# Performance work log

Measured on AMD Instinct MI355X. Metric: run time of the kernel, lower is better.

## Reference

```python
import jax, jax.numpy as jnp
import numpy as np

N, E = 100000, 1600000
IN_D, BOND_D, HID, OUT_D = 64, 16, 128, 64
COMB = 2 * IN_D + BOND_D + 1  # 145


def _mlp(h, W1, b1, W2, b2):
    # Linear -> SiLU -> Linear
    h = h @ W1 + b1
    h = jax.nn.silu(h)
    return h @ W2 + b2


def setup_inputs() -> dict:
    key = jax.random.key(0)
    ks = jax.random.split(key, 16)
    s = 0.05
    return {
        "x": jax.random.normal(ks[0], (N, IN_D), dtype=jnp.float32),
        "pos": jax.random.normal(ks[1], (N, 3), dtype=jnp.float32),
        "edge_attr": jax.random.normal(ks[2], (E, BOND_D), dtype=jnp.float32),
        "edge_index": jax.random.randint(ks[3], (2, E), 0, N, dtype=jnp.int64),
        # phi_x
        "W1x": jax.random.normal(ks[4], (COMB, HID), dtype=jnp.float32) * s,
        "b1x": jnp.zeros((HID,), jnp.float32),
        "W2x": jax.random.normal(ks[5], (HID, OUT_D), dtype=jnp.float32) * s,
        "b2x": jnp.zeros((OUT_D,), jnp.float32),
        # phi_pos
        "W1p": jax.random.normal(ks[6], (COMB, HID), dtype=jnp.float32) * s,
        "b1p": jnp.zeros((HID,), jnp.float32),
        "W2p": jax.random.normal(ks[7], (HID, 1), dtype=jnp.float32) * s,
        "b2p": jnp.zeros((1,), jnp.float32),
        # phi_edge
        "W1e": jax.random.normal(ks[8], (COMB, HID), dtype=jnp.float32) * s,
        "b1e": jnp.zeros((HID,), jnp.float32),
        "W2e": jax.random.normal(ks[9], (HID, BOND_D), dtype=jnp.float32) * s,
        "b2e": jnp.zeros((BOND_D,), jnp.float32),
    }


def reference(x, pos, edge_attr, edge_index,
              W1x, b1x, W2x, b2x,
              W1p, b1p, W2p, b2p,
              W1e, b1e, W2e, b2e):
    row, col = edge_index[0], edge_index[1]
    rel_pos = pos[row] - pos[col]                      # [E, 3]
    dist_sq = jnp.sum(rel_pos ** 2, axis=-1, keepdims=True)  # [E, 1]
    combined = jnp.concatenate([x[row], x[col], edge_attr, dist_sq], axis=-1)  # [E, COMB]

    msg_x = _mlp(combined, W1x, b1x, W2x, b2x)         # [E, OUT_D]
    aggregated_x = jnp.zeros_like(x).at[col].add(msg_x)

    weight_pos = _mlp(combined, W1p, b1p, W2p, b2p)    # [E, 1]
    pos_update = weight_pos * rel_pos                  # [E, 3]
    aggregated_pos = jnp.zeros_like(pos).at[col].add(pos_update)

    edge_update = _mlp(combined, W1e, b1e, W2e, b2e)   # [E, BOND_D]
    return aggregated_x, aggregated_pos, edge_update
```

## Files before the change

kernel.cpp:

```cpp
#include <hip/hip_runtime.h>

typedef __bf16 bf16_t;
typedef __bf16 bf16x8 __attribute__((ext_vector_type(8)));
typedef float f32x4 __attribute__((ext_vector_type(4)));
typedef float f32x16 __attribute__((ext_vector_type(16)));

#define TILE_E 64
#define CSTR 168
#define HSTR 136

#define W2X_OFF (120 * 512)
#define W2P_OFF (136 * 512)
#define W2E_OFF (140 * 512)
#define XBF_OFF (144 * 512)

__global__ void prep_w(const float* __restrict__ W1x, const float* __restrict__ b1x,
                       const float* __restrict__ W1p, const float* __restrict__ b1p,
                       const float* __restrict__ W1e, const float* __restrict__ b1e,
                       const float* __restrict__ W2x, const float* __restrict__ W2p,
                       const float* __restrict__ W2e, bf16_t* __restrict__ wf)
{
    const int cid = blockIdx.x;
    const int lane = threadIdx.x;
    float v[8];
    if (cid < 120) {
        const int m = cid / 40, rem = cid % 40, ct = rem / 10, kk = rem % 10;
        const float* W1 = (m == 0) ? W1x : ((m == 1) ? W1p : W1e);
        const float* b1 = (m == 0) ? b1x : ((m == 1) ? b1p : b1e);
        const int n = ct * 32 + (lane & 31);
        const int kb = kk * 16 + (lane >> 5) * 8;
#pragma unroll
        for (int j = 0; j < 8; ++j) {
            const int k = kb + j;
            v[j] = (k < 145) ? W1[k * 128 + n] : ((k == 145) ? b1[n] : 0.0f);
        }
    } else if (cid < 136) {
        const int c2 = cid - 120, ct2 = c2 / 8, kk = c2 % 8;
        const int n = ct2 * 32 + (lane & 31);
        const int kb = kk * 16 + (lane >> 5) * 8;
#pragma unroll
        for (int j = 0; j < 8; ++j) v[j] = W2x[(kb + j) * 64 + n];
    } else if (cid < 140) {
        const int kk = cid - 136;
        const int n = lane & 15;
        const int kb = kk * 32 + (lane >> 4) * 8;
#pragma unroll
        for (int j = 0; j < 8; ++j) v[j] = (n == 0) ? W2p[kb + j] : 0.0f;
    } else {
        const int kk = cid - 140;
        const int n = lane & 15;
        const int kb = kk * 32 + (lane >> 4) * 8;
#pragma unroll
        for (int j = 0; j < 8; ++j) v[j] = W2e[(kb + j) * 16 + n];
    }
    bf16x8 o;
#pragma unroll
    for (int j = 0; j < 8; ++j) o[j] = (bf16_t)v[j];
    *(bf16x8*)(wf + (long)cid * 512 + lane * 8) = o;
}

__global__ void prep_x_kernel(const float* __restrict__ x, bf16_t* __restrict__ xbf, int n8)
{
    const int i = blockIdx.x * blockDim.x + threadIdx.x;
    if (i < n8) {
        const float4* p = (const float4*)x + (long)i * 2;
        float4 a = p[0], b = p[1];
        bf16x8 v;
        v[0] = (bf16_t)a.x; v[1] = (bf16_t)a.y; v[2] = (bf16_t)a.z; v[3] = (bf16_t)a.w;
        v[4] = (bf16_t)b.x; v[5] = (bf16_t)b.y; v[6] = (bf16_t)b.z; v[7] = (bf16_t)b.w;
        ((bf16x8*)xbf)[i] = v;
    }
}

__global__ __launch_bounds__(256, 3)
void egnn_main(const float* __restrict__ x, const float* __restrict__ pos,
               const float* __restrict__ ea, const int* __restrict__ eidx,
               const float* __restrict__ b2x, const float* __restrict__ b2p,
               const float* __restrict__ b2e,
               const bf16_t* __restrict__ wf, const bf16_t* __restrict__ xbf,
               float* __restrict__ aggx, float* __restrict__ aggpos,
               float* __restrict__ eup, int N, int E)
{
    __shared__ __align__(16) bf16_t s_comb[TILE_E * CSTR];
    __shared__ __align__(16) bf16_t s_H[TILE_E * HSTR];
    __shared__ float s_rel[TILE_E][3];
    __shared__ int s_col[TILE_E];

    const int tid = threadIdx.x;
    const int lane = tid & 63;
    const int wv = tid >> 6;
    const long e0 = (long)blockIdx.x * TILE_E;

    if (tid < TILE_E) {
        long e = e0 + tid;
        int r = 0, c = 0;
        if (e < E) { r = eidx[e]; c = eidx[(long)E + e]; }
        s_col[tid] = c;
        float ax = 0.f, ay = 0.f, az = 0.f;
        if (e < E) {
            const float* pr = pos + (long)r * 3;
            const float* pc = pos + (long)c * 3;
            ax = pr[0] - pc[0]; ay = pr[1] - pc[1]; az = pr[2] - pc[2];
        }
        s_rel[tid][0] = ax; s_rel[tid][1] = ay; s_rel[tid][2] = az;
        bf16_t* cr = s_comb + tid * CSTR;
        cr[144] = (bf16_t)(ax * ax + ay * ay + az * az);
        cr[145] = (bf16_t)1.0f;
#pragma unroll
        for (int p = 146; p < 160; ++p) cr[p] = (bf16_t)0.0f;
    }

    {
        const int el = tid >> 2, q = tid & 3;
        long e = e0 + el;
        int r = 0, c = 0;
        if (e < E) { r = eidx[e]; c = eidx[(long)E + e]; }
        bf16_t* dst = s_comb + el * CSTR;
        if (xbf) {
            const uint4* pr = (const uint4*)(xbf + (long)r * 64) + q * 2;
            const uint4* pc = (const uint4*)(xbf + (long)c * 64) + q * 2;
            uint4 a0 = pr[0], a1 = pr[1], c0 = pc[0], c1 = pc[1];
            uint4* d0 = (uint4*)(dst + q * 16);
            d0[0] = a0; d0[1] = a1;
            uint4* d1 = (uint4*)(dst + 64 + q * 16);
            d1[0] = c0; d1[1] = c1;
        } else {
            const float4* pr = (const float4*)(x + (long)r * 64) + q * 4;
            const float4* pc = (const float4*)(x + (long)c * 64) + q * 4;
            bf16_t* d0 = dst + q * 16;
            bf16_t* d1 = dst + 64 + q * 16;
#pragma unroll
            for (int i = 0; i < 4; ++i) {
                float4 v = pr[i];
                d0[i * 4 + 0] = (bf16_t)v.x; d0[i * 4 + 1] = (bf16_t)v.y;
                d0[i * 4 + 2] = (bf16_t)v.z; d0[i * 4 + 3] = (bf16_t)v.w;
            }
#pragma unroll
            for (int i = 0; i < 4; ++i) {
                float4 v = pc[i];
                d1[i * 4 + 0] = (bf16_t)v.x; d1[i * 4 + 1] = (bf16_t)v.y;
                d1[i * 4 + 2] = (bf16_t)v.z; d1[i * 4 + 3] = (bf16_t)v.w;
            }
        }
        float4 v = {0.f, 0.f, 0.f, 0.f};
        if (e < E) v = ((const float4*)(ea + (long)e * 16))[q];
        bf16_t* da = dst + 128 + q * 4;
        da[0] = (bf16_t)v.x; da[1] = (bf16_t)v.y; da[2] = (bf16_t)v.z; da[3] = (bf16_t)v.w;
    }
    __syncthreads();

    for (int m = 0; m < 3; ++m) {
        f32x16 acc0 = {0.0f};
        f32x16 acc1 = {0.0f};
        {
            const bf16_t* bb = wf + (long)((m * 4 + wv) * 10) * 512 + lane * 8;
            bf16x8 B[10];
#pragma unroll
            for (int kk = 0; kk < 10; ++kk) B[kk] = *(const bf16x8*)(bb + kk * 512);
            const bf16_t* ar0 = s_comb + (lane & 31) * CSTR + (lane >> 5) * 8;
            const bf16_t* ar1 = ar0 + 32 * CSTR;
#pragma unroll
            for (int kk = 0; kk < 10; ++kk) {
                bf16x8 a0 = *(const bf16x8*)(ar0 + kk * 16);
                bf16x8 a1 = *(const bf16x8*)(ar1 + kk * 16);
                acc0 = __builtin_amdgcn_mfma_f32_32x32x16_bf16(a0, B[kk], acc0, 0, 0, 0);
                acc1 = __builtin_amdgcn_mfma_f32_32x32x16_bf16(a1, B[kk], acc1, 0, 0, 0);
            }
        }
        {
            const int col = wv * 32 + (lane & 31);
            const int rbase = 4 * (lane >> 5);
#pragma unroll
            for (int g = 0; g < 16; ++g) {
                const int row = rbase + (g & 3) + 8 * (g >> 2);
                float h = acc0[g];
                float s = h * __builtin_amdgcn_rcpf(1.0f + __builtin_amdgcn_exp2f(-1.44269504f * h));
                s_H[row * HSTR + col] = (bf16_t)s;
            }
#pragma unroll
            for (int g = 0; g < 16; ++g) {
                const int row = 32 + rbase + (g & 3) + 8 * (g >> 2);
                float h = acc1[g];
                float s = h * __builtin_amdgcn_rcpf(1.0f + __builtin_amdgcn_exp2f(-1.44269504f * h));
                s_H[row * HSTR + col] = (bf16_t)s;
            }
        }
        __syncthreads();

        if (m == 0) {
            const int ct2 = wv & 1, rt = wv >> 1;
            f32x16 acc = {0.0f};
            const bf16_t* bb = wf + W2X_OFF + (long)(ct2 * 8) * 512 + lane * 8;
            const bf16_t* ar = s_H + (rt * 32 + (lane & 31)) * HSTR + (lane >> 5) * 8;
#pragma unroll
            for (int kk = 0; kk < 8; ++kk) {
                bf16x8 a = *(const bf16x8*)(ar + kk * 16);
                bf16x8 b = *(const bf16x8*)(bb + kk * 512);
                acc = __builtin_amdgcn_mfma_f32_32x32x16_bf16(a, b, acc, 0, 0, 0);
            }
            const int oc = ct2 * 32 + (lane & 31);
            const float bias = b2x[oc];
            const int rb = rt * 32 + 4 * (lane >> 5);
#pragma unroll
            for (int g = 0; g < 16; ++g) {
                const int row = rb + (g & 3) + 8 * (g >> 2);
                long e = e0 + row;
                if (e < E) atomicAdd(aggx + (long)s_col[row] * 64 + oc, acc[g] + bias);
            }
        } else if (m == 1) {
            f32x4 acc = {0.0f};
            const bf16_t* bb = wf + W2P_OFF + lane * 8;
            const bf16_t* ar = s_H + (wv * 16 + (lane & 15)) * HSTR + (lane >> 4) * 8;
#pragma unroll
            for (int kk = 0; kk < 4; ++kk) {
                bf16x8 a = *(const bf16x8*)(ar + kk * 32);
                bf16x8 b = *(const bf16x8*)(bb + kk * 512);
                acc = __builtin_amdgcn_mfma_f32_16x16x32_bf16(a, b, acc, 0, 0, 0);
            }
            if ((lane & 15) == 0) {
                const float bias = b2p[0];
#pragma unroll
                for (int j = 0; j < 4; ++j) {
                    const int row = wv * 16 + (lane >> 4) * 4 + j;
                    long e = e0 + row;
                    if (e < E) {
                        const float w = acc[j] + bias;
                        const long c3 = (long)s_col[row] * 3;
                        atomicAdd(aggpos + c3 + 0, w * s_rel[row][0]);
                        atomicAdd(aggpos + c3 + 1, w * s_rel[row][1]);
                        atomicAdd(aggpos + c3 + 2, w * s_rel[row][2]);
                    }
                }
            }
        } else {
            f32x4 acc = {0.0f};
            const bf16_t* bb = wf + W2E_OFF + lane * 8;
            const bf16_t* ar = s_H + (wv * 16 + (lane & 15)) * HSTR + (lane >> 4) * 8;
#pragma unroll
            for (int kk = 0; kk < 4; ++kk) {
                bf16x8 a = *(const bf16x8*)(ar + kk * 32);
                bf16x8 b = *(const bf16x8*)(bb + kk * 512);
                acc = __builtin_amdgcn_mfma_f32_16x16x32_bf16(a, b, acc, 0, 0, 0);
            }
            const float bias = b2e[lane & 15];
#pragma unroll
            for (int j = 0; j < 4; ++j) {
                const int row = wv * 16 + (lane >> 4) * 4 + j;
                long e = e0 + row;
                if (e < E) eup[e * 16 + (lane & 15)] = acc[j] + bias;
            }
        }
        __syncthreads();
    }
}

extern "C" void kernel_launch(void* const* d_in, const int* in_sizes, int n_in,
                              void* d_out, int out_size, void* d_ws, size_t ws_size,
                              hipStream_t stream)
{
    const float* x   = (const float*)d_in[0];
    const float* pos = (const float*)d_in[1];
    const float* ea  = (const float*)d_in[2];
    const int*   eidx= (const int*)d_in[3];
    const float* W1x = (const float*)d_in[4];
    const float* b1x = (const float*)d_in[5];
    const float* W2x = (const float*)d_in[6];
    const float* b2x = (const float*)d_in[7];
    const float* W1p = (const float*)d_in[8];
    const float* b1p = (const float*)d_in[9];
    const float* W2p = (const float*)d_in[10];
    const float* b2p = (const float*)d_in[11];
    const float* W1e = (const float*)d_in[12];
    const float* b1e = (const float*)d_in[13];
    const float* W2e = (const float*)d_in[14];
    const float* b2e = (const float*)d_in[15];

    const int N = in_sizes[0] / 64;
    const int E = in_sizes[2] / 16;

    bf16_t* wf = (bf16_t*)d_ws;
    const size_t need_xbf = (size_t)XBF_OFF * 2 + (size_t)N * 64 * 2;
    bf16_t* xbf = (ws_size >= need_xbf) ? (wf + XBF_OFF) : nullptr;

    float* aggx = (float*)d_out;
    float* aggp = aggx + (long)N * 64;
    float* eup  = aggp + (long)N * 3;

    hipMemsetAsync(d_out, 0, (size_t)(N * 64 + N * 3) * sizeof(float), stream);

    hipLaunchKernelGGL(prep_w, dim3(144), dim3(64), 0, stream,
                       W1x, b1x, W1p, b1p, W1e, b1e, W2x, W2p, W2e, wf);
    if (xbf) {
        const int n8 = (N * 64) / 8;
        hipLaunchKernelGGL(prep_x_kernel, dim3((n8 + 255) / 256), dim3(256), 0, stream,
                           x, xbf, n8);
    }
    const int tiles = (E + TILE_E - 1) / TILE_E;
    hipLaunchKernelGGL(egnn_main, dim3(tiles), dim3(256), 0, stream,
                       x, pos, ea, eidx, b2x, b2p, b2e, wf, xbf, aggx, aggp, eup, N, E);
}
```

Measured before the change: 872.6 us.

## Fuse three hidden-layer GEMMs into one pass and split output MLPs across waves

```diff
diff --git a/kernel.cpp b/kernel.cpp
--- a/kernel.cpp
+++ b/kernel.cpp
@@ -7,7 +7,7 @@
 
 #define TILE_E 64
 #define CSTR 168
-#define HSTR 136
+#define HS2  392
 
 #define W2X_OFF (120 * 512)
 #define W2P_OFF (136 * 512)
@@ -24,10 +24,11 @@
     const int lane = threadIdx.x;
     float v[8];
     if (cid < 120) {
-        const int m = cid / 40, rem = cid % 40, ct = rem / 10, kk = rem % 10;
+        const int ctg = cid / 10, kk = cid % 10;
+        const int m = ctg >> 2;
         const float* W1 = (m == 0) ? W1x : ((m == 1) ? W1p : W1e);
         const float* b1 = (m == 0) ? b1x : ((m == 1) ? b1p : b1e);
-        const int n = ct * 32 + (lane & 31);
+        const int n = (ctg & 3) * 32 + (lane & 31);
         const int kb = kk * 16 + (lane >> 5) * 8;
 #pragma unroll
         for (int j = 0; j < 8; ++j) {
@@ -81,8 +82,7 @@
                float* __restrict__ aggx, float* __restrict__ aggpos,
                float* __restrict__ eup, int N, int E)
 {
-    __shared__ __align__(16) bf16_t s_comb[TILE_E * CSTR];
-    __shared__ __align__(16) bf16_t s_H[TILE_E * HSTR];
+    __shared__ __align__(16) bf16_t s_buf[TILE_E * HS2];
     __shared__ float s_rel[TILE_E][3];
     __shared__ int s_col[TILE_E];
 
@@ -103,7 +103,7 @@
             ax = pr[0] - pc[0]; ay = pr[1] - pc[1]; az = pr[2] - pc[2];
         }
         s_rel[tid][0] = ax; s_rel[tid][1] = ay; s_rel[tid][2] = az;
-        bf16_t* cr = s_comb + tid * CSTR;
+        bf16_t* cr = s_buf + tid * CSTR;
         cr[144] = (bf16_t)(ax * ax + ay * ay + az * az);
         cr[145] = (bf16_t)1.0f;
 #pragma unroll
@@ -115,7 +115,7 @@
         long e = e0 + el;
         int r = 0, c = 0;
         if (e < E) { r = eidx[e]; c = eidx[(long)E + e]; }
-        bf16_t* dst = s_comb + el * CSTR;
+        bf16_t* dst = s_buf + el * CSTR;
         if (xbf) {
             const uint4* pr = (const uint4*)(xbf + (long)r * 64) + q * 2;
             const uint4* pc = (const uint4*)(xbf + (long)c * 64) + q * 2;
@@ -149,82 +149,95 @@
     }
     __syncthreads();
 
-    for (int m = 0; m < 3; ++m) {
-        f32x16 acc0 = {0.0f};
-        f32x16 acc1 = {0.0f};
-        {
-            const bf16_t* bb = wf + (long)((m * 4 + wv) * 10) * 512 + lane * 8;
+    f32x16 acc[3][2] = {};
+    {
+        const bf16_t* ar0 = s_buf + (lane & 31) * CSTR + (lane >> 5) * 8;
+        const bf16_t* ar1 = ar0 + 32 * CSTR;
+#pragma unroll
+        for (int ct = 0; ct < 3; ++ct) {
+            const bf16_t* bb = wf + (long)((wv * 3 + ct) * 10) * 512 + lane * 8;
             bf16x8 B[10];
 #pragma unroll
             for (int kk = 0; kk < 10; ++kk) B[kk] = *(const bf16x8*)(bb + kk * 512);
-            const bf16_t* ar0 = s_comb + (lane & 31) * CSTR + (lane >> 5) * 8;
-            const bf16_t* ar1 = ar0 + 32 * CSTR;
 #pragma unroll
             for (int kk = 0; kk < 10; ++kk) {
                 bf16x8 a0 = *(const bf16x8*)(ar0 + kk * 16);
                 bf16x8 a1 = *(const bf16x8*)(ar1 + kk * 16);
-                acc0 = __builtin_amdgcn_mfma_f32_32x32x16_bf16(a0, B[kk], acc0, 0, 0, 0);
-                acc1 = __builtin_amdgcn_mfma_f32_32x32x16_bf16(a1, B[kk], acc1, 0, 0, 0);
-            }
-        }
-        {
-            const int col = wv * 32 + (lane & 31);
-            const int rbase = 4 * (lane >> 5);
-#pragma unroll
-            for (int g = 0; g < 16; ++g) {
-                const int row = rbase + (g & 3) + 8 * (g >> 2);
-                float h = acc0[g];
-                float s = h * __builtin_amdgcn_rcpf(1.0f + __builtin_amdgcn_exp2f(-1.44269504f * h));
-                s_H[row * HSTR + col] = (bf16_t)s;
-            }
-#pragma unroll
-            for (int g = 0; g < 16; ++g) {
-                const int row = 32 + rbase + (g & 3) + 8 * (g >> 2);
-                float h = acc1[g];
-                float s = h * __builtin_amdgcn_rcpf(1.0f + __builtin_amdgcn_exp2f(-1.44269504f * h));
-                s_H[row * HSTR + col] = (bf16_t)s;
-            }
-        }
-        __syncthreads();
-
-        if (m == 0) {
-            const int ct2 = wv & 1, rt = wv >> 1;
-            f32x16 acc = {0.0f};
-            const bf16_t* bb = wf + W2X_OFF + (long)(ct2 * 8) * 512 + lane * 8;
-            const bf16_t* ar = s_H + (rt * 32 + (lane & 31)) * HSTR + (lane >> 5) * 8;
-#pragma unroll
-            for (int kk = 0; kk < 8; ++kk) {
-                bf16x8 a = *(const bf16x8*)(ar + kk * 16);
-                bf16x8 b = *(const bf16x8*)(bb + kk * 512);
-                acc = __builtin_amdgcn_mfma_f32_32x32x16_bf16(a, b, acc, 0, 0, 0);
-            }
-            const int oc = ct2 * 32 + (lane & 31);
-            const float bias = b2x[oc];
-            const int rb = rt * 32 + 4 * (lane >> 5);
-#pragma unroll
-            for (int g = 0; g < 16; ++g) {
-                const int row = rb + (g & 3) + 8 * (g >> 2);
-                long e = e0 + row;
-                if (e < E) atomicAdd(aggx + (long)s_col[row] * 64 + oc, acc[g] + bias);
-            }
-        } else if (m == 1) {
-            f32x4 acc = {0.0f};
-            const bf16_t* bb = wf + W2P_OFF + lane * 8;
-            const bf16_t* ar = s_H + (wv * 16 + (lane & 15)) * HSTR + (lane >> 4) * 8;
+                acc[ct][0] = __builtin_amdgcn_mfma_f32_32x32x16_bf16(a0, B[kk], acc[ct][0], 0, 0, 0);
+                acc[ct][1] = __builtin_amdgcn_mfma_f32_32x32x16_bf16(a1, B[kk], acc[ct][1], 0, 0, 0);
+            }
+        }
+    }
+    __syncthreads();
+
+    {
+        const int rbase = 4 * (lane >> 5);
+#pragma unroll
+        for (int ct = 0; ct < 3; ++ct) {
+            const int col = (wv * 3 + ct) * 32 + (lane & 31);
+#pragma unroll
+            for (int half = 0; half < 2; ++half) {
+#pragma unroll
+                for (int g = 0; g < 16; ++g) {
+                    const int row = half * 32 + rbase + (g & 3) + 8 * (g >> 2);
+                    float h = acc[ct][half][g];
+                    float s = h * __builtin_amdgcn_rcpf(1.0f + __builtin_amdgcn_exp2f(-1.44269504f * h));
+                    s_buf[row * HS2 + col] = (bf16_t)s;
+                }
+            }
+        }
+    }
+    __syncthreads();
+
+    if (wv < 2) {
+        f32x16 a0 = {0.0f}, a1 = {0.0f};
+        const bf16_t* bb = wf + W2X_OFF + (long)(wv * 8) * 512 + lane * 8;
+        const bf16_t* ar = s_buf + (lane & 31) * HS2 + (lane >> 5) * 8;
+#pragma unroll
+        for (int kk = 0; kk < 8; ++kk) {
+            bf16x8 b = *(const bf16x8*)(bb + kk * 512);
+            bf16x8 av0 = *(const bf16x8*)(ar + kk * 16);
+            bf16x8 av1 = *(const bf16x8*)(ar + 32 * HS2 + kk * 16);
+            a0 = __builtin_amdgcn_mfma_f32_32x32x16_bf16(av0, b, a0, 0, 0, 0);
+            a1 = __builtin_amdgcn_mfma_f32_32x32x16_bf16(av1, b, a1, 0, 0, 0);
+        }
+        const int oc = wv * 32 + (lane & 31);
+        const float bias = b2x[oc];
+        const int rb = 4 * (lane >> 5);
+#pragma unroll
+        for (int g = 0; g < 16; ++g) {
+            const int row = rb + (g & 3) + 8 * (g >> 2);
+            long e = e0 + row;
+            if (e < E) atomicAdd(aggx + (long)s_col[row] * 64 + oc, a0[g] + bias);
+        }
+#pragma unroll
+        for (int g = 0; g < 16; ++g) {
+            const int row = 32 + rb + (g & 3) + 8 * (g >> 2);
+            long e = e0 + row;
+            if (e < E) atomicAdd(aggx + (long)s_col[row] * 64 + oc, a1[g] + bias);
+        }
+    } else if (wv == 2) {
+        const bf16_t* bb = wf + W2P_OFF + lane * 8;
+        bf16x8 Bp[4];
+#pragma unroll
+        for (int kk = 0; kk < 4; ++kk) Bp[kk] = *(const bf16x8*)(bb + kk * 512);
+        const float bias = b2p[0];
+#pragma unroll
+        for (int rt = 0; rt < 4; ++rt) {
+            f32x4 acc4 = {0.0f};
+            const bf16_t* ar = s_buf + (rt * 16 + (lane & 15)) * HS2 + 128 + (lane >> 4) * 8;
 #pragma unroll
             for (int kk = 0; kk < 4; ++kk) {
                 bf16x8 a = *(const bf16x8*)(ar + kk * 32);
-                bf16x8 b = *(const bf16x8*)(bb + kk * 512);
-                acc = __builtin_amdgcn_mfma_f32_16x16x32_bf16(a, b, acc, 0, 0, 0);
+                acc4 = __builtin_amdgcn_mfma_f32_16x16x32_bf16(a, Bp[kk], acc4, 0, 0, 0);
             }
             if ((lane & 15) == 0) {
-                const float bias = b2p[0];
 #pragma unroll
                 for (int j = 0; j < 4; ++j) {
-                    const int row = wv * 16 + (lane >> 4) * 4 + j;
+                    const int row = rt * 16 + (lane >> 4) * 4 + j;
                     long e = e0 + row;
                     if (e < E) {
-                        const float w = acc[j] + bias;
+                        const float w = acc4[j] + bias;
                         const long c3 = (long)s_col[row] * 3;
                         atomicAdd(aggpos + c3 + 0, w * s_rel[row][0]);
                         atomicAdd(aggpos + c3 + 1, w * s_rel[row][1]);
@@ -232,25 +245,29 @@
                     }
                 }
             }
-        } else {
-            f32x4 acc = {0.0f};
-            const bf16_t* bb = wf + W2E_OFF + lane * 8;
-            const bf16_t* ar = s_H + (wv * 16 + (lane & 15)) * HSTR + (lane >> 4) * 8;
+        }
+    } else {
+        const bf16_t* bb = wf + W2E_OFF + lane * 8;
+        bf16x8 Be[4];
+#pragma unroll
+        for (int kk = 0; kk < 4; ++kk) Be[kk] = *(const bf16x8*)(bb + kk * 512);
+        const float bias = b2e[lane & 15];
+#pragma unroll
+        for (int rt = 0; rt < 4; ++rt) {
+            f32x4 acc4 = {0.0f};
+            const bf16_t* ar = s_buf + (rt * 16 + (lane & 15)) * HS2 + 256 + (lane >> 4) * 8;
 #pragma unroll
             for (int kk = 0; kk < 4; ++kk) {
                 bf16x8 a = *(const bf16x8*)(ar + kk * 32);
-                bf16x8 b = *(const bf16x8*)(bb + kk * 512);
-                acc = __builtin_amdgcn_mfma_f32_16x16x32_bf16(a, b, acc, 0, 0, 0);
-            }
-            const float bias = b2e[lane & 15];
+                acc4 = __builtin_amdgcn_mfma_f32_16x16x32_bf16(a, Be[kk], acc4, 0, 0, 0);
+            }
 #pragma unroll
             for (int j = 0; j < 4; ++j) {
-                const int row = wv * 16 + (lane >> 4) * 4 + j;
+                const int row = rt * 16 + (lane >> 4) * 4 + j;
                 long e = e0 + row;
-                if (e < E) eup[e * 16 + (lane & 15)] = acc[j] + bias;
-            }
-        }
-        __syncthreads();
+                if (e < E) eup[e * 16 + (lane & 15)] = acc4[j] + bias;
+            }
+        }
     }
 }
 
```

Result: slower. 1.102 ms (+26.3%).
